# Kernel optimization log

Hardware: AMD Instinct MI355X
Metric: run time of the kernel (lower is better)

The kernel has to match this reference:

```python
import jax, jax.numpy as jnp
import numpy as np

EPS = 1e-12      # torch F.normalize eps
NEG = -9999.0    # masked score fill value (as in source)
BETA_P = 0.1

def _l2norm(x):
    n = jnp.linalg.norm(x, axis=-1, keepdims=True)
    return x / jnp.maximum(n, EPS)

def setup_inputs() -> dict:
    key = jax.random.key(0)
    k0, k1, k2, k3 = jax.random.split(key, 4)
    B, Lq, Ld, D, NWAY = 64, 32, 256, 128, 8
    query_reps = jax.random.normal(k0, (B, Lq, D), jnp.float32)
    doc_reps = jax.random.normal(k1, (B, NWAY, Ld, D), jnp.float32)
    doc_masks = jax.random.randint(k2, (B, NWAY, Ld), 0, 2).astype(jnp.int32)
    doc_masks = doc_masks.at[..., 0].set(1)  # ensure each doc has >=1 valid token
    # labels: [B, 2*nway] = [teacher log-probs | binary positive mask]
    teacher = jax.nn.log_softmax(jax.random.normal(k3, (B, NWAY), jnp.float32), axis=-1)
    wmask = jnp.zeros((B, NWAY), jnp.float32).at[:, 0].set(1.0)
    labels = jnp.concatenate([teacher, wmask], axis=1)
    return {"query_reps": query_reps, "doc_reps": doc_reps,
            "doc_masks": doc_masks, "labels": labels}

def reference(query_reps, doc_reps, doc_masks, labels):
    # query_reps [B,Lq,D], doc_reps [B,N,Ld,D], doc_masks [B,N,Ld], labels [B,2N]
    q = _l2norm(query_reps)                                   # [B,Lq,D]
    m = doc_masks.astype(doc_reps.dtype)
    d = _l2norm(doc_reps * m[..., None])                      # [B,N,Ld,D]
    s = jnp.einsum('bqe,bnke->bnqk', q, d)                    # [B,N,Lq,Ld]
    s = jnp.where(doc_masks[:, :, None, :] == 0, NEG, s)
    scores = s.max(axis=-1).sum(axis=-1)                      # maxsim -> [B,N]
    log_scores = jax.nn.log_softmax(scores, axis=-1)
    nway = labels.shape[1] // 2
    target = labels[:, :nway]
    wmasks = labels[:, nway:]
    # KLDivLoss(reduction='none', log_target=True): exp(t) * (t - input)
    losses = jnp.exp(target) * (target - log_scores)
    loss_pos = -jnp.sum(log_scores * wmasks)
    return jnp.mean(losses) + BETA_P * loss_pos
```

## Files before the change

### kernel.cpp

```cpp
#include <hip/hip_runtime.h>
#include <hip/hip_bf16.h>

#define NB 64
#define LQ 32
#define LD 256
#define DD 128
#define NWAY 8
#define KT 64
#define LDSROW 136

typedef __attribute__((ext_vector_type(8))) short short8;
typedef __attribute__((ext_vector_type(4))) float f32x4;

static __device__ __forceinline__ unsigned short f2bf(float f) {
    unsigned int u = __float_as_uint(f);
    u += 0x7fffu + ((u >> 16) & 1u);
    return (unsigned short)(u >> 16);
}
static __device__ __forceinline__ unsigned int pk2(float a, float b) {
    return (unsigned int)f2bf(a) | ((unsigned int)f2bf(b) << 16);
}

__global__ __launch_bounds__(512, 4) void colbert_scores_kernel(
    const float* __restrict__ qreps,
    const float* __restrict__ dreps,
    const int*   __restrict__ masks,
    float*       __restrict__ scores)
{
    const int bid  = blockIdx.x;
    const int b    = bid & 63;
    const int n    = bid >> 6;
    const int bn   = b * NWAY + n;
    const int tid  = threadIdx.x;
    const int lane = tid & 63;
    const int w    = tid >> 6;

    __shared__ __align__(16) unsigned short qs[LQ * LDSROW];
    __shared__ __align__(16) unsigned short dsb[2][KT * LDSROW];
    __shared__ float rnds[2][KT];
    __shared__ int   mks[LD];
    __shared__ float qmaxs[4][LQ];

    if (tid >= 256) {
        const int i = tid - 256;
        mks[i] = masks[(size_t)bn * LD + i];
    } else {
        const int qrow = tid >> 3, qseg = tid & 7;
        const float* src = qreps + ((size_t)b * LQ + qrow) * DD + qseg * 16;
        float4 q0 = reinterpret_cast<const float4*>(src)[0];
        float4 q1 = reinterpret_cast<const float4*>(src)[1];
        float4 q2 = reinterpret_cast<const float4*>(src)[2];
        float4 q3 = reinterpret_cast<const float4*>(src)[3];
        float ss = q0.x*q0.x + q0.y*q0.y + q0.z*q0.z + q0.w*q0.w
                 + q1.x*q1.x + q1.y*q1.y + q1.z*q1.z + q1.w*q1.w
                 + q2.x*q2.x + q2.y*q2.y + q2.z*q2.z + q2.w*q2.w
                 + q3.x*q3.x + q3.y*q3.y + q3.z*q3.z + q3.w*q3.w;
        ss += __shfl_xor(ss, 1); ss += __shfl_xor(ss, 2); ss += __shfl_xor(ss, 4);
        const float rn = rsqrtf(fmaxf(ss, 1e-24f));
        unsigned int qp[8] = {
            pk2(q0.x*rn, q0.y*rn), pk2(q0.z*rn, q0.w*rn),
            pk2(q1.x*rn, q1.y*rn), pk2(q1.z*rn, q1.w*rn),
            pk2(q2.x*rn, q2.y*rn), pk2(q2.z*rn, q2.w*rn),
            pk2(q3.x*rn, q3.y*rn), pk2(q3.z*rn, q3.w*rn) };
        unsigned short* dst = &qs[qrow * LDSROW + qseg * 16];
        reinterpret_cast<uint4*>(dst)[0] = *reinterpret_cast<const uint4*>(&qp[0]);
        reinterpret_cast<uint4*>(dst)[1] = *reinterpret_cast<const uint4*>(&qp[4]);
    }
    __syncthreads();

    const int row = tid >> 3;
    const int seg = tid & 7;
    float va[16], vb[16];

    auto prefetch = [&](float (&v)[16], int t) {
        if (mks[t * KT + row]) {
            const float* src = dreps + ((size_t)bn * LD + t * KT + row) * DD + seg * 16;
            #pragma unroll
            for (int i = 0; i < 4; ++i) {
                float4 f = reinterpret_cast<const float4*>(src)[i];
                v[4*i] = f.x; v[4*i+1] = f.y; v[4*i+2] = f.z; v[4*i+3] = f.w;
            }
        }
    };
    auto stagewrite = [&](float (&v)[16], int t, int bf) {
        if (mks[t * KT + row]) {
            unsigned int dp[8];
            #pragma unroll
            for (int i = 0; i < 8; ++i) dp[i] = pk2(v[2*i], v[2*i+1]);
            unsigned short* dst = &dsb[bf][row * LDSROW + seg * 16];
            reinterpret_cast<uint4*>(dst)[0] = *reinterpret_cast<const uint4*>(&dp[0]);
            reinterpret_cast<uint4*>(dst)[1] = *reinterpret_cast<const uint4*>(&dp[4]);
            float ss = 0.f;
            #pragma unroll
            for (int i = 0; i < 16; ++i) ss += v[i] * v[i];
            ss += __shfl_xor(ss, 1); ss += __shfl_xor(ss, 2); ss += __shfl_xor(ss, 4);
            if (seg == 0) rnds[bf][row] = rsqrtf(fmaxf(ss, 1e-24f));
        }
    };

    const int frow  = lane & 15;
    const int fpack = lane >> 4;
    const int qh    = w & 1;
    const int kq    = w >> 1;
    const unsigned short* aptr = &qs[(qh * 16 + frow) * LDSROW + fpack * 8];

    float rmax[4] = {-1e30f, -1e30f, -1e30f, -1e30f};

    auto mfma_max = [&](int t, int bf) {
        const int drow = kq * 16 + frow;
        const unsigned short* bptr = &dsb[bf][drow * LDSROW + fpack * 8];
        f32x4 acc = {0.f, 0.f, 0.f, 0.f};
        #pragma unroll
        for (int kc = 0; kc < 4; ++kc) {
            short8 a  = *reinterpret_cast<const short8*>(aptr + kc * 32);
            short8 bb = *reinterpret_cast<const short8*>(bptr + kc * 32);
            acc = __builtin_amdgcn_mfma_f32_16x16x32_bf16(a, bb, acc, 0, 0, 0);
        }
        if (mks[t * KT + drow]) {
            const float rnd = rnds[bf][drow];
            #pragma unroll
            for (int r = 0; r < 4; ++r) rmax[r] = fmaxf(rmax[r], acc[r] * rnd);
        }
    };

    prefetch(va, 0);  prefetch(vb, 1);
    stagewrite(va, 0, 0);
    __syncthreads();
    prefetch(va, 2);
    mfma_max(0, 0);
    stagewrite(vb, 1, 1);
    __syncthreads();
    prefetch(vb, 3);
    mfma_max(1, 1);
    stagewrite(va, 2, 0);
    __syncthreads();
    mfma_max(2, 0);
    stagewrite(vb, 3, 1);
    __syncthreads();
    mfma_max(3, 1);

    #pragma unroll
    for (int r = 0; r < 4; ++r) {
        float m = rmax[r];
        m = fmaxf(m, __shfl_xor(m, 1));
        m = fmaxf(m, __shfl_xor(m, 2));
        m = fmaxf(m, __shfl_xor(m, 4));
        m = fmaxf(m, __shfl_xor(m, 8));
        rmax[r] = m;
    }
    if ((lane & 15) == 0) {
        const int qr = qh * 16 + fpack * 4;
        #pragma unroll
        for (int r = 0; r < 4; ++r) qmaxs[kq][qr + r] = rmax[r];
    }
    __syncthreads();

    if (w == 0) {
        float s = 0.f;
        if (lane < 32)
            s = fmaxf(fmaxf(qmaxs[0][lane], qmaxs[1][lane]),
                      fmaxf(qmaxs[2][lane], qmaxs[3][lane]));
        s += __shfl_xor(s, 1);  s += __shfl_xor(s, 2);  s += __shfl_xor(s, 4);
        s += __shfl_xor(s, 8);  s += __shfl_xor(s, 16); s += __shfl_xor(s, 32);
        if (lane == 0) scores[bn] = s;
    }
}

__global__ __launch_bounds__(64) void colbert_loss_kernel(
    const float* __restrict__ scores,
    const float* __restrict__ labels,
    float*       __restrict__ out)
{
    const int b = threadIdx.x;
    float sc[NWAY];
    float m = -1e30f;
    #pragma unroll
    for (int j = 0; j < NWAY; ++j) { sc[j] = scores[b * NWAY + j]; m = fmaxf(m, sc[j]); }
    float se = 0.f;
    #pragma unroll
    for (int j = 0; j < NWAY; ++j) se += expf(sc[j] - m);
    const float lse = m + logf(se);

    float lossb = 0.f, posb = 0.f;
    #pragma unroll
    for (int j = 0; j < NWAY; ++j) {
        const float ls = sc[j] - lse;
        const float tg = labels[b * 2 * NWAY + j];
        const float wv = labels[b * 2 * NWAY + NWAY + j];
        lossb += expf(tg) * (tg - ls);
        posb  += ls * wv;
    }
    float a = lossb, p = posb;
    #pragma unroll
    for (int d = 1; d < 64; d <<= 1) { a += __shfl_xor(a, d); p += __shfl_xor(p, d); }
    if (b == 0) out[0] = a / 512.0f - 0.1f * p;
}

extern "C" void kernel_launch(void* const* d_in, const int* in_sizes, int n_in,
                              void* d_out, int out_size, void* d_ws, size_t ws_size,
                              hipStream_t stream) {
    const float* qreps  = (const float*)d_in[0];
    const float* dreps  = (const float*)d_in[1];
    const int*   masks  = (const int*)d_in[2];
    const float* labels = (const float*)d_in[3];
    float* scores = (float*)d_ws;
    float* out    = (float*)d_out;

    colbert_scores_kernel<<<NB * NWAY, 512, 0, stream>>>(qreps, dreps, masks, scores);
    colbert_loss_kernel<<<1, 64, 0, stream>>>(scores, labels, out);
}
```

Before: 16.00 us.

## Fuse loss into scores kernel via last-block atomic counter, keep masks in registers

Merges the separate loss kernel into the scores kernel. Each block publishes its score with a release store and bumps a global atomic counter, and the last block to finish computes the log-softmax/KL loss. Each thread also loads its four mask values straight into registers, which removes the first __syncthreads before prefetch. This saves one kernel launch but adds a hipMemsetAsync to reset the counter and an atomic per block.

New measurement: 31.73 us. 98.3% more time.

```diff
diff --git a/kernel.cpp b/kernel.cpp
--- a/kernel.cpp
+++ b/kernel.cpp
@@ -7,6 +7,7 @@
 #define DD 128
 #define NWAY 8
 #define KT 64
+#define NBLOCKS (NB * NWAY)
 #define LDSROW 136
 
 typedef __attribute__((ext_vector_type(8))) short short8;
@@ -21,11 +22,14 @@
     return (unsigned int)f2bf(a) | ((unsigned int)f2bf(b) << 16);
 }
 
-__global__ __launch_bounds__(512, 4) void colbert_scores_kernel(
+__global__ __launch_bounds__(512, 4) void colbert_fused_kernel(
     const float* __restrict__ qreps,
     const float* __restrict__ dreps,
     const int*   __restrict__ masks,
-    float*       __restrict__ scores)
+    const float* __restrict__ labels,
+    float*       __restrict__ scores,
+    unsigned*    __restrict__ cnt,
+    float*       __restrict__ out)
 {
     const int bid  = blockIdx.x;
     const int b    = bid & 63;
@@ -40,6 +44,15 @@
     __shared__ float rnds[2][KT];
     __shared__ int   mks[LD];
     __shared__ float qmaxs[4][LQ];
+    __shared__ unsigned islast;
+
+    const int row = tid >> 3;
+    const int seg = tid & 7;
+
+    int mymask[4];
+    #pragma unroll
+    for (int t = 0; t < 4; ++t)
+        mymask[t] = masks[(size_t)bn * LD + t * KT + row];
 
     if (tid >= 256) {
         const int i = tid - 256;
@@ -66,14 +79,11 @@
         reinterpret_cast<uint4*>(dst)[0] = *reinterpret_cast<const uint4*>(&qp[0]);
         reinterpret_cast<uint4*>(dst)[1] = *reinterpret_cast<const uint4*>(&qp[4]);
     }
-    __syncthreads();
-
-    const int row = tid >> 3;
-    const int seg = tid & 7;
+
     float va[16], vb[16];
 
     auto prefetch = [&](float (&v)[16], int t) {
-        if (mks[t * KT + row]) {
+        if (mymask[t]) {
             const float* src = dreps + ((size_t)bn * LD + t * KT + row) * DD + seg * 16;
             #pragma unroll
             for (int i = 0; i < 4; ++i) {
@@ -83,7 +93,7 @@
         }
     };
     auto stagewrite = [&](float (&v)[16], int t, int bf) {
-        if (mks[t * KT + row]) {
+        if (mymask[t]) {
             unsigned int dp[8];
             #pragma unroll
             for (int i = 0; i < 8; ++i) dp[i] = pk2(v[2*i], v[2*i+1]);
@@ -162,38 +172,44 @@
                       fmaxf(qmaxs[2][lane], qmaxs[3][lane]));
         s += __shfl_xor(s, 1);  s += __shfl_xor(s, 2);  s += __shfl_xor(s, 4);
         s += __shfl_xor(s, 8);  s += __shfl_xor(s, 16); s += __shfl_xor(s, 32);
-        if (lane == 0) scores[bn] = s;
-    }
-}
-
-__global__ __launch_bounds__(64) void colbert_loss_kernel(
-    const float* __restrict__ scores,
-    const float* __restrict__ labels,
-    float*       __restrict__ out)
-{
-    const int b = threadIdx.x;
-    float sc[NWAY];
-    float m = -1e30f;
-    #pragma unroll
-    for (int j = 0; j < NWAY; ++j) { sc[j] = scores[b * NWAY + j]; m = fmaxf(m, sc[j]); }
-    float se = 0.f;
-    #pragma unroll
-    for (int j = 0; j < NWAY; ++j) se += expf(sc[j] - m);
-    const float lse = m + logf(se);
-
-    float lossb = 0.f, posb = 0.f;
-    #pragma unroll
-    for (int j = 0; j < NWAY; ++j) {
-        const float ls = sc[j] - lse;
-        const float tg = labels[b * 2 * NWAY + j];
-        const float wv = labels[b * 2 * NWAY + NWAY + j];
-        lossb += expf(tg) * (tg - ls);
-        posb  += ls * wv;
-    }
-    float a = lossb, p = posb;
-    #pragma unroll
-    for (int d = 1; d < 64; d <<= 1) { a += __shfl_xor(a, d); p += __shfl_xor(p, d); }
-    if (b == 0) out[0] = a / 512.0f - 0.1f * p;
+        if (lane == 0) {
+            __hip_atomic_store(&scores[bn], s, __ATOMIC_RELEASE, __HIP_MEMORY_SCOPE_AGENT);
+            unsigned old = __hip_atomic_fetch_add(cnt, 1u, __ATOMIC_ACQ_REL,
+                                                  __HIP_MEMORY_SCOPE_AGENT);
+            islast = (old == NBLOCKS - 1) ? 1u : 0u;
+        }
+    }
+    __syncthreads();
+
+    if (islast && tid < 64) {
+        const int bb = tid;
+        float sc[NWAY];
+        float m = -1e30f;
+        #pragma unroll
+        for (int j = 0; j < NWAY; ++j) {
+            sc[j] = __hip_atomic_load(&scores[bb * NWAY + j],
+                                      __ATOMIC_ACQUIRE, __HIP_MEMORY_SCOPE_AGENT);
+            m = fmaxf(m, sc[j]);
+        }
+        float se = 0.f;
+        #pragma unroll
+        for (int j = 0; j < NWAY; ++j) se += expf(sc[j] - m);
+        const float lse = m + logf(se);
+
+        float lossb = 0.f, posb = 0.f;
+        #pragma unroll
+        for (int j = 0; j < NWAY; ++j) {
+            const float ls = sc[j] - lse;
+            const float tg = labels[bb * 2 * NWAY + j];
+            const float wv = labels[bb * 2 * NWAY + NWAY + j];
+            lossb += expf(tg) * (tg - ls);
+            posb  += ls * wv;
+        }
+        float a = lossb, p = posb;
+        #pragma unroll
+        for (int d = 1; d < 64; d <<= 1) { a += __shfl_xor(a, d); p += __shfl_xor(p, d); }
+        if (tid == 0) out[0] = a / 512.0f - 0.1f * p;
+    }
 }
 
 extern "C" void kernel_launch(void* const* d_in, const int* in_sizes, int n_in,
@@ -203,9 +219,11 @@
     const float* dreps  = (const float*)d_in[1];
     const int*   masks  = (const int*)d_in[2];
     const float* labels = (const float*)d_in[3];
-    float* scores = (float*)d_ws;
-    float* out    = (float*)d_out;
-
-    colbert_scores_kernel<<<NB * NWAY, 512, 0, stream>>>(qreps, dreps, masks, scores);
-    colbert_loss_kernel<<<1, 64, 0, stream>>>(scores, labels, out);
-}
+    float*    scores = (float*)d_ws;
+    unsigned* cnt    = (unsigned*)((char*)d_ws + NBLOCKS * sizeof(float));
+    float*    out    = (float*)d_out;
+
+    hipMemsetAsync(cnt, 0, sizeof(unsigned), stream);
+    colbert_fused_kernel<<<NBLOCKS, 512, 0, stream>>>(qreps, dreps, masks, labels,
+                                                      scores, cnt, out);
+}
```

## Load whole doc tile into LDS at once, drop double-buffered pipeline

Applied to the files above, without the earlier changes.

Each thread now issues all of its global loads for the full 256-row document up front (two threads per row, 64 floats each) and stages the whole tile in dynamic LDS as bf16, replacing the 4-stage double-buffered prefetch with four barriers. Query fragments are hoisted into registers once, and mask values for the MFMA columns are read straight from global memory into registers. This removes intermediate barriers and puts more memory requests in flight early, at the cost of about 79KB of LDS and 64 floats of registers per thread, which lowers occupancy. It also adds a dead loop and a per-launch hipFuncSetAttribute call.

Result: no change. 16.27 us (+1.7%).

```diff
diff --git a/kernel.cpp b/kernel.cpp
--- a/kernel.cpp
+++ b/kernel.cpp
@@ -6,8 +6,9 @@
 #define LD 256
 #define DD 128
 #define NWAY 8
-#define KT 64
-#define LDSROW 136
+#define NBLOCKS (NB * NWAY)
+#define DSROW 136
+#define SMEM_BYTES ((256 + 32) * DSROW * 2 + 256 * 4 + 128 * 4)
 
 typedef __attribute__((ext_vector_type(8))) short short8;
 typedef __attribute__((ext_vector_type(4))) float f32x4;
@@ -27,6 +28,12 @@
     const int*   __restrict__ masks,
     float*       __restrict__ scores)
 {
+    extern __shared__ unsigned short smem[];
+    unsigned short* ds_  = smem;
+    unsigned short* qs   = smem + 256 * DSROW;
+    float*          rnds = (float*)(smem + (256 + 32) * DSROW);
+    float*          qmaxs = rnds + 256;
+
     const int bid  = blockIdx.x;
     const int b    = bid & 63;
     const int n    = bid >> 6;
@@ -34,17 +41,30 @@
     const int tid  = threadIdx.x;
     const int lane = tid & 63;
     const int w    = tid >> 6;
-
-    __shared__ __align__(16) unsigned short qs[LQ * LDSROW];
-    __shared__ __align__(16) unsigned short dsb[2][KT * LDSROW];
-    __shared__ float rnds[2][KT];
-    __shared__ int   mks[LD];
-    __shared__ float qmaxs[4][LQ];
-
-    if (tid >= 256) {
-        const int i = tid - 256;
-        mks[i] = masks[(size_t)bn * LD + i];
-    } else {
+    const int fr   = lane & 15;
+    const int fp   = lane >> 4;
+    const int qh   = w & 1;
+    const int kq   = w >> 1;
+
+    const int row  = tid >> 1;
+    const int half = tid & 1;
+
+    const int rm = masks[(size_t)bn * LD + row];
+    int cm[4];
+    #pragma unroll
+    for (int tt = 0; tt < 4; ++tt)
+        cm[tt] = masks[(size_t)bn * LD + tt * 64 + kq * 16 + fr];
+
+    float4 fa[8], fb[8];
+    const float* dsrc = dreps + ((size_t)bn * LD + row) * DD + half * 64;
+    if (rm) {
+        #pragma unroll
+        for (int i = 0; i < 8; ++i) fa[i] = reinterpret_cast<const float4*>(dsrc)[i];
+        #pragma unroll
+        for (int i = 0; i < 8; ++i) fb[i] = reinterpret_cast<const float4*>(dsrc + 32)[i];
+    }
+
+    if (tid < 256) {
         const int qrow = tid >> 3, qseg = tid & 7;
         const float* src = qreps + ((size_t)b * LQ + qrow) * DD + qseg * 16;
         float4 q0 = reinterpret_cast<const float4*>(src)[0];
@@ -62,82 +82,71 @@
             pk2(q1.x*rn, q1.y*rn), pk2(q1.z*rn, q1.w*rn),
             pk2(q2.x*rn, q2.y*rn), pk2(q2.z*rn, q2.w*rn),
             pk2(q3.x*rn, q3.y*rn), pk2(q3.z*rn, q3.w*rn) };
-        unsigned short* dst = &qs[qrow * LDSROW + qseg * 16];
+        unsigned short* dst = &qs[qrow * DSROW + qseg * 16];
         reinterpret_cast<uint4*>(dst)[0] = *reinterpret_cast<const uint4*>(&qp[0]);
         reinterpret_cast<uint4*>(dst)[1] = *reinterpret_cast<const uint4*>(&qp[4]);
     }
+
+    if (rm) {
+        float ss = 0.f;
+        #pragma unroll
+        for (int i = 0; i < 8; ++i)
+            ss += fa[i].x*fa[i].x + fa[i].y*fa[i].y + fa[i].z*fa[i].z + fa[i].w*fa[i].w
+                + fb[i].x*fb[i].x + fb[i].y*fb[i].y + fb[i].z*fb[i].z + fb[i].w*fb[i].w;
+        ss += __shfl_xor(ss, 1);
+        const float rn = rsqrtf(fmaxf(ss, 1e-24f));
+        if (half == 0) rnds[row] = rn;
+
+        unsigned short* dst = &ds_[row * DSROW + half * 64];
+        #pragma unroll
+        for (int i = 0; i < 8; ++i) {
+            unsigned int dp[4] = { pk2(fa[i].x, fa[i].y), pk2(fa[i].z, fa[i].w),
+                                   0u, 0u };
+            dp[2] = 0u; dp[3] = 0u;
+            (void)dp;
+            break;
+        }
+        #pragma unroll
+        for (int i = 0; i < 4; ++i) {
+            unsigned int dp[4] = {
+                pk2(fa[2*i].x, fa[2*i].y),   pk2(fa[2*i].z, fa[2*i].w),
+                pk2(fa[2*i+1].x, fa[2*i+1].y), pk2(fa[2*i+1].z, fa[2*i+1].w) };
+            reinterpret_cast<uint4*>(dst)[i] = *reinterpret_cast<const uint4*>(dp);
+        }
+        #pragma unroll
+        for (int i = 0; i < 4; ++i) {
+            unsigned int dp[4] = {
+                pk2(fb[2*i].x, fb[2*i].y),   pk2(fb[2*i].z, fb[2*i].w),
+                pk2(fb[2*i+1].x, fb[2*i+1].y), pk2(fb[2*i+1].z, fb[2*i+1].w) };
+            reinterpret_cast<uint4*>(dst + 32)[i] = *reinterpret_cast<const uint4*>(dp);
+        }
+    }
+
     __syncthreads();
 
-    const int row = tid >> 3;
-    const int seg = tid & 7;
-    float va[16], vb[16];
-
-    auto prefetch = [&](float (&v)[16], int t) {
-        if (mks[t * KT + row]) {
-            const float* src = dreps + ((size_t)bn * LD + t * KT + row) * DD + seg * 16;
-            #pragma unroll
-            for (int i = 0; i < 4; ++i) {
-                float4 f = reinterpret_cast<const float4*>(src)[i];
-                v[4*i] = f.x; v[4*i+1] = f.y; v[4*i+2] = f.z; v[4*i+3] = f.w;
-            }
-        }
-    };
-    auto stagewrite = [&](float (&v)[16], int t, int bf) {
-        if (mks[t * KT + row]) {
-            unsigned int dp[8];
-            #pragma unroll
-            for (int i = 0; i < 8; ++i) dp[i] = pk2(v[2*i], v[2*i+1]);
-            unsigned short* dst = &dsb[bf][row * LDSROW + seg * 16];
-            reinterpret_cast<uint4*>(dst)[0] = *reinterpret_cast<const uint4*>(&dp[0]);
-            reinterpret_cast<uint4*>(dst)[1] = *reinterpret_cast<const uint4*>(&dp[4]);
-            float ss = 0.f;
-            #pragma unroll
-            for (int i = 0; i < 16; ++i) ss += v[i] * v[i];
-            ss += __shfl_xor(ss, 1); ss += __shfl_xor(ss, 2); ss += __shfl_xor(ss, 4);
-            if (seg == 0) rnds[bf][row] = rsqrtf(fmaxf(ss, 1e-24f));
-        }
-    };
-
-    const int frow  = lane & 15;
-    const int fpack = lane >> 4;
-    const int qh    = w & 1;
-    const int kq    = w >> 1;
-    const unsigned short* aptr = &qs[(qh * 16 + frow) * LDSROW + fpack * 8];
+    short8 afr[4];
+    const unsigned short* ap = &qs[(qh * 16 + fr) * DSROW + fp * 8];
+    #pragma unroll
+    for (int kc = 0; kc < 4; ++kc)
+        afr[kc] = *reinterpret_cast<const short8*>(ap + kc * 32);
 
     float rmax[4] = {-1e30f, -1e30f, -1e30f, -1e30f};
-
-    auto mfma_max = [&](int t, int bf) {
-        const int drow = kq * 16 + frow;
-        const unsigned short* bptr = &dsb[bf][drow * LDSROW + fpack * 8];
+    #pragma unroll
+    for (int tt = 0; tt < 4; ++tt) {
+        const int drow = tt * 64 + kq * 16 + fr;
+        const unsigned short* bp = &ds_[drow * DSROW + fp * 8];
         f32x4 acc = {0.f, 0.f, 0.f, 0.f};
         #pragma unroll
         for (int kc = 0; kc < 4; ++kc) {
-            short8 a  = *reinterpret_cast<const short8*>(aptr + kc * 32);
-            short8 bb = *reinterpret_cast<const short8*>(bptr + kc * 32);
-            acc = __builtin_amdgcn_mfma_f32_16x16x32_bf16(a, bb, acc, 0, 0, 0);
-        }
-        if (mks[t * KT + drow]) {
-            const float rnd = rnds[bf][drow];
+            short8 bb = *reinterpret_cast<const short8*>(bp + kc * 32);
+            acc = __builtin_amdgcn_mfma_f32_16x16x32_bf16(afr[kc], bb, acc, 0, 0, 0);
+        }
+        if (cm[tt]) {
+            const float rnd = rnds[drow];
             #pragma unroll
             for (int r = 0; r < 4; ++r) rmax[r] = fmaxf(rmax[r], acc[r] * rnd);
         }
-    };
-
-    prefetch(va, 0);  prefetch(vb, 1);
-    stagewrite(va, 0, 0);
-    __syncthreads();
-    prefetch(va, 2);
-    mfma_max(0, 0);
-    stagewrite(vb, 1, 1);
-    __syncthreads();
-    prefetch(vb, 3);
-    mfma_max(1, 1);
-    stagewrite(va, 2, 0);
-    __syncthreads();
-    mfma_max(2, 0);
-    stagewrite(vb, 3, 1);
-    __syncthreads();
-    mfma_max(3, 1);
+    }
 
     #pragma unroll
     for (int r = 0; r < 4; ++r) {
@@ -148,18 +157,18 @@
         m = fmaxf(m, __shfl_xor(m, 8));
         rmax[r] = m;
     }
-    if ((lane & 15) == 0) {
-        const int qr = qh * 16 + fpack * 4;
-        #pragma unroll
-        for (int r = 0; r < 4; ++r) qmaxs[kq][qr + r] = rmax[r];
+    if (fr == 0) {
+        #pragma unroll
+        for (int r = 0; r < 4; ++r)
+            qmaxs[kq * 32 + qh * 16 + fp * 4 + r] = rmax[r];
     }
     __syncthreads();
 
     if (w == 0) {
         float s = 0.f;
         if (lane < 32)
-            s = fmaxf(fmaxf(qmaxs[0][lane], qmaxs[1][lane]),
-                      fmaxf(qmaxs[2][lane], qmaxs[3][lane]));
+            s = fmaxf(fmaxf(qmaxs[0 * 32 + lane], qmaxs[1 * 32 + lane]),
+                      fmaxf(qmaxs[2 * 32 + lane], qmaxs[3 * 32 + lane]));
         s += __shfl_xor(s, 1);  s += __shfl_xor(s, 2);  s += __shfl_xor(s, 4);
         s += __shfl_xor(s, 8);  s += __shfl_xor(s, 16); s += __shfl_xor(s, 32);
         if (lane == 0) scores[bn] = s;
@@ -203,9 +212,12 @@
     const float* dreps  = (const float*)d_in[1];
     const int*   masks  = (const int*)d_in[2];
     const float* labels = (const float*)d_in[3];
-    float* scores = (float*)d_ws;
-    float* out    = (float*)d_out;
-
-    colbert_scores_kernel<<<NB * NWAY, 512, 0, stream>>>(qreps, dreps, masks, scores);
-    colbert_loss_kernel<<<1, 64, 0, stream>>>(scores, labels, out);
-}
+    float* scoresp = (float*)d_ws;
+    float* out     = (float*)d_out;
+
+    hipFuncSetAttribute((const void*)colbert_scores_kernel,
+                        hipFuncAttributeMaxDynamicSharedMemorySize, SMEM_BYTES);
+
+    colbert_scores_kernel<<<NBLOCKS, 512, SMEM_BYTES, stream>>>(qreps, dreps, masks, scoresp);
+    colbert_loss_kernel<<<1, 64, 0, stream>>>(scoresp, labels, out);
+}
```
